# Performance work log

Measured on AMD Instinct MI355X. Metric: run time of the kernel, lower is better.

## Reference

```python
import jax, jax.numpy as jnp
import numpy as np

SIGMA_DATA = 16.0
ALPHA_BOND = 1.0


def safe_norm(x, axis=-1):
    # L2 norm with zero (sub)gradient at 0, matching torch.norm's behavior
    sq = jnp.sum(x * x, axis=axis)
    n = jnp.sqrt(jnp.where(sq > 0, sq, 1.0))
    return jnp.where(sq > 0, n, 0.0)


def weighted_rigid_align(x_l, xGT_l, w_l):
    # Aligns x_l onto xGT_l's frame (Kabsch with weights); output is detached.
    wm = w_l[..., None]                                   # [B,N,1]
    denom = jnp.sum(wm, axis=1, keepdims=True)
    mu = jnp.sum(wm * x_l, axis=1, keepdims=True) / denom
    muGT = jnp.sum(wm * xGT_l, axis=1, keepdims=True) / denom
    xc = x_l - mu
    xGTc = xGT_l - muGT
    # M = (w * xGT_c)^T @ x_c  -> [B,3,3]
    M = jnp.einsum('bni,bnj->bij', wm * xGTc, xc)
    U, S, Vh = jnp.linalg.svd(M)
    R = U @ Vh
    det = jnp.linalg.det(R)
    Fm = jnp.array([[1.0, 0.0, 0.0], [0.0, 1.0, 0.0], [0.0, 0.0, -1.0]], dtype=R.dtype)
    Rfix = jnp.einsum('bij,jk,bkl->bil', U, Fm, Vh)
    R = jnp.where(det[:, None, None] < 0, Rfix, R)
    xalign = xc @ jnp.swapaxes(R, -1, -2) + muGT
    return jax.lax.stop_gradient(xalign)


def diffusion_loss(xpred_l, xGT_l, ht, w_l):
    # Align ground truth onto prediction (note arg order in original forward)
    xGT_aligned = weighted_rigid_align(xGT_l, xpred_l, w_l)
    loss = jnp.sum(safe_norm(xpred_l - xGT_aligned) * w_l) / jnp.sum(w_l)
    if ALPHA_BOND > 0:
        w_pair = w_l[:, :, None] * w_l[:, None, :]                 # [B,N,N]
        d_pred = safe_norm(xpred_l[:, :, None] - xpred_l[:, None]) # [B,N,N]
        d_gt = safe_norm(xGT_l[:, :, None] - xGT_l[:, None])       # [B,N,N]
        L_bond = w_pair * (d_pred - d_gt) ** 2
        loss = loss + ALPHA_BOND * jnp.sum(L_bond) / jnp.sum(w_pair)
    return (ht ** 2 + SIGMA_DATA ** 2) / (ht + SIGMA_DATA) ** 2 * loss


def setup_inputs() -> dict:
    key = jax.random.key(0)
    k1, k2, k3, k4 = jax.random.split(key, 4)
    B, N = 4, 2048
    xpred_l = jax.random.normal(k1, (B, N, 3), dtype=jnp.float32) * 10.0
    xGT_l = jax.random.normal(k2, (B, N, 3), dtype=jnp.float32) * 10.0
    ht = jax.random.uniform(k3, (B,), dtype=jnp.float32, minval=0.1, maxval=4.0)
    w_l = jax.random.uniform(k4, (B, N), dtype=jnp.float32, minval=0.1, maxval=1.0)
    return {"xpred_l": xpred_l, "xGT_l": xGT_l, "ht": ht, "w_l": w_l}


def reference(xpred_l, xGT_l, ht, w_l):
    return diffusion_loss(xpred_l, xGT_l, ht, w_l)
```

## Files before the change

### kernel.cpp

```cpp
#include <hip/hip_runtime.h>
#include <math.h>


#define RT 256
#define CT 64
#define MAXB 8
#define MAXGX 16

__global__ __launch_bounds__(RT, 4)
void k_bond_stats(const float* __restrict__ pred, const float* __restrict__ gt,
                  const float* __restrict__ w, double* __restrict__ ws,
                  int N, int B) {
    const int b    = blockIdx.z;
    const int bx   = blockIdx.x;
    const int r0   = bx * RT;
    const int c0   = blockIdx.y * CT;
    const int tid  = threadIdx.x;
    const int lane = tid & 63, wave = tid >> 6;
    const int GX   = gridDim.x;
    const unsigned linear = (blockIdx.z * gridDim.y + blockIdx.y) * GX + blockIdx.x;

    double* statsSlot = ws;
    double* bondSlot  = ws + (size_t)B * GX * 16;

    const float* p  = pred + (size_t)b * N * 3;
    const float* g  = gt   + (size_t)b * N * 3;
    const float* wb = w    + (size_t)b * N;

    __shared__ float4 sp4[CT], sg4[CT];
    __shared__ double shred[4][16];

    const int  n      = r0 + tid;
    const bool row_ok = (n < N);
    float px=0.f,py=0.f,pz=0.f,gx=0.f,gy=0.f,gz=0.f,wn=0.f;
    if (row_ok) {
        px = p[3*n]; py = p[3*n+1]; pz = p[3*n+2];
        gx = g[3*n]; gy = g[3*n+1]; gz = g[3*n+2];
        wn = wb[n];
    }

    const bool bond_active = (c0 + CT > r0 + 1) && (c0 < N);
    float bond_f = 0.0f;
    if (bond_active) {
        for (int i = tid; i < CT; i += RT) {
            int m = c0 + i;
            float4 a = make_float4(0.f,0.f,0.f,0.f), c = a;
            if (m < N) {
                a = make_float4(p[3*m], p[3*m+1], p[3*m+2], wb[m]);
                c = make_float4(g[3*m], g[3*m+1], g[3*m+2], 0.f);
            }
            sp4[i] = a; sg4[i] = c;
        }
        __syncthreads();
        if (row_ok) {
            const int cc = min(CT, N - c0);
            if (c0 >= r0 + RT) {
                #pragma unroll 4
                for (int i = 0; i < cc; i++) {
                    float4 cp = sp4[i], cg = sg4[i];
                    float dxp=px-cp.x, dyp=py-cp.y, dzp=pz-cp.z;
                    float dxg=gx-cg.x, dyg=gy-cg.y, dzg=gz-cg.z;
                    float dp = sqrtf(dxp*dxp+dyp*dyp+dzp*dzp);
                    float dg = sqrtf(dxg*dxg+dyg*dyg+dzg*dzg);
                    float dd = dp - dg;
                    bond_f += (wn*cp.w)*(dd*dd);
                }
            } else if (n < c0 + cc - 1) {
                #pragma unroll 4
                for (int i = 0; i < cc; i++) {
                    float4 cp = sp4[i], cg = sg4[i];
                    float dxp=px-cp.x, dyp=py-cp.y, dzp=pz-cp.z;
                    float dxg=gx-cg.x, dyg=gy-cg.y, dzg=gz-cg.z;
                    float dp = sqrtf(dxp*dxp+dyp*dyp+dzp*dzp);
                    float dg = sqrtf(dxg*dxg+dyg*dyg+dzg*dzg);
                    float dd = dp - dg;
                    float t  = (wn*cp.w)*(dd*dd);
                    bond_f += (c0 + i > n) ? t : 0.0f;
                }
            }
        }
    }
    bond_f *= 2.0f;

    if (blockIdx.y == 0) {
        double wd=wn, pxd=px,pyd=py,pzd=pz, gxd=gx,gyd=gy,gzd=gz;
        double st[16] = {wd, wd*pxd, wd*pyd, wd*pzd, wd*gxd, wd*gyd, wd*gzd,
                         wd*pxd*gxd, wd*pxd*gyd, wd*pxd*gzd,
                         wd*pyd*gxd, wd*pyd*gyd, wd*pyd*gzd,
                         wd*pzd*gxd, wd*pzd*gyd, wd*pzd*gzd};
        #pragma unroll
        for (int off = 32; off > 0; off >>= 1) {
            #pragma unroll
            for (int k = 0; k < 16; k++) st[k] += __shfl_down(st[k], off, 64);
        }
        if (lane == 0) {
            #pragma unroll
            for (int k = 0; k < 16; k++) shred[wave][k] = st[k];
        }
        __syncthreads();
        if (tid < 16)
            statsSlot[((size_t)b*GX + bx)*16 + tid] =
                shred[0][tid]+shred[1][tid]+shred[2][tid]+shred[3][tid];
        __syncthreads();
    }

    double bd = (double)bond_f;
    #pragma unroll
    for (int off = 32; off > 0; off >>= 1) bd += __shfl_down(bd, off, 64);
    if (lane == 0) shred[wave][0] = bd;
    __syncthreads();
    if (tid == 0)
        bondSlot[linear] = shred[0][0]+shred[1][0]+shred[2][0]+shred[3][0];
}

__global__ __launch_bounds__(RT, 1)
void k_tail(const float* __restrict__ pred, const float* __restrict__ gt,
            const float* __restrict__ ht, const float* __restrict__ w,
            float* __restrict__ out, const double* __restrict__ ws,
            int N, int B, int GX, unsigned total) {
    const int tid  = threadIdx.x;
    const int lane = tid & 63, wave = tid >> 6;
    const double* statsSlot = ws;
    const double* bondSlot  = ws + (size_t)B * GX * 16;

    __shared__ double sstat[MAXB][16];
    __shared__ double shred[4][16];
    __shared__ float  Rf[MAXB][15];
    __shared__ double Wd[MAXB];
    __shared__ double s_bond, s_loss;

    if (tid < B * 16) {
        int bb = tid >> 4, k = tid & 15;
        double acc = 0.0;
        for (int j = 0; j < GX; j++) acc += statsSlot[((size_t)bb*GX + j)*16 + k];
        sstat[bb][k] = acc;
    }

    double bsum = 0.0;
    for (unsigned i = tid; i < total; i += RT) bsum += bondSlot[i];
    #pragma unroll
    for (int off = 32; off > 0; off >>= 1) bsum += __shfl_down(bsum, off, 64);
    if (lane == 0) shred[wave][0] = bsum;
    __syncthreads();
    if (tid == 0) s_bond = shred[0][0]+shred[1][0]+shred[2][0]+shred[3][0];

    if (tid < B) {
        const double* s = sstat[tid];
        double W = s[0];
        double mup[3] = { s[1]/W, s[2]/W, s[3]/W };
        double mug[3] = { s[4]/W, s[5]/W, s[6]/W };
        double M[3][3];
        for (int i = 0; i < 3; i++)
            for (int j = 0; j < 3; j++)
                M[i][j] = s[7 + i*3 + j] - W * mup[i] * mug[j];
        double A[3][3];
        for (int i = 0; i < 3; i++)
            for (int j = 0; j < 3; j++) {
                double t = 0.0;
                for (int k = 0; k < 3; k++) t += M[k][i] * M[k][j];
                A[i][j] = t;
            }
        double V[3][3] = {{1,0,0},{0,1,0},{0,0,1}};
        for (int sweep = 0; sweep < 6; sweep++) {
            for (int pq = 0; pq < 3; pq++) {
                int pp_ = (pq == 2) ? 1 : 0;
                int qq_ = (pq == 0) ? 1 : 2;
                double apq = A[pp_][qq_];
                if (fabs(apq) < 1e-300) continue;
                double app = A[pp_][pp_], aqq = A[qq_][qq_];
                double theta = (aqq - app) / (2.0 * apq);
                double t = copysign(1.0, theta) / (fabs(theta) + sqrt(theta*theta + 1.0));
                double cj = 1.0 / sqrt(t*t + 1.0), sn = t * cj;
                A[pp_][pp_] = app - t * apq;
                A[qq_][qq_] = aqq + t * apq;
                A[pp_][qq_] = A[qq_][pp_] = 0.0;
                int r = 3 - pp_ - qq_;
                double arp = A[r][pp_], arq = A[r][qq_];
                A[r][pp_] = A[pp_][r] = cj*arp - sn*arq;
                A[r][qq_] = A[qq_][r] = sn*arp + cj*arq;
                for (int rr = 0; rr < 3; rr++) {
                    double vp = V[rr][pp_], vq = V[rr][qq_];
                    V[rr][pp_] = cj*vp - sn*vq;
                    V[rr][qq_] = sn*vp + cj*vq;
                }
            }
        }
        double d[3] = { A[0][0], A[1][1], A[2][2] };
        int idx[3] = {0, 1, 2};
        for (int i = 0; i < 2; i++)
            for (int j = i + 1; j < 3; j++)
                if (d[idx[j]] > d[idx[i]]) { int tt = idx[i]; idx[i] = idx[j]; idx[j] = tt; }
        double u[3][3], v[3][3];
        for (int i = 0; i < 3; i++) {
            int c_ = idx[i];
            double sv = sqrt(fmax(d[c_], 0.0));
            double inv = (sv > 1e-12) ? 1.0 / sv : 0.0;
            for (int r = 0; r < 3; r++) v[i][r] = V[r][c_];
            for (int r = 0; r < 3; r++) {
                double t = 0.0;
                for (int k = 0; k < 3; k++) t += M[r][k] * v[i][k];
                u[i][r] = t * inv;
            }
        }
        double detM = M[0][0]*(M[1][1]*M[2][2] - M[1][2]*M[2][1])
                    - M[0][1]*(M[1][0]*M[2][2] - M[1][2]*M[2][0])
                    + M[0][2]*(M[1][0]*M[2][1] - M[1][1]*M[2][0]);
        double sg2 = (detM < 0.0) ? -1.0 : 1.0;
        for (int r = 0; r < 3; r++)
            for (int cc2 = 0; cc2 < 3; cc2++)
                Rf[tid][r*3+cc2] = (float)(u[0][r]*v[0][cc2] + u[1][r]*v[1][cc2]
                                           + sg2 * u[2][r]*v[2][cc2]);
        for (int i = 0; i < 3; i++) Rf[tid][9 + i]  = (float)mup[i];
        for (int i = 0; i < 3; i++) Rf[tid][12 + i] = (float)mug[i];
        Wd[tid] = W;
    }
    __syncthreads();

    double al = 0.0;
    for (int bb = 0; bb < B; bb++) {
        float R0=Rf[bb][0], R1=Rf[bb][1], R2=Rf[bb][2];
        float R3=Rf[bb][3], R4=Rf[bb][4], R5=Rf[bb][5];
        float R6=Rf[bb][6], R7=Rf[bb][7], R8=Rf[bb][8];
        float mp0=Rf[bb][9],  mp1=Rf[bb][10], mp2=Rf[bb][11];
        float mg0=Rf[bb][12], mg1=Rf[bb][13], mg2=Rf[bb][14];
        const float* pp  = pred + (size_t)bb * N * 3;
        const float* gg  = gt   + (size_t)bb * N * 3;
        const float* wwb = w    + (size_t)bb * N;
        for (int nn = tid; nn < N; nn += RT) {
            float x0 = gg[3*nn]-mg0, x1 = gg[3*nn+1]-mg1, x2 = gg[3*nn+2]-mg2;
            float ax = fmaf(R0,x0, fmaf(R1,x1, fmaf(R2,x2, mp0)));
            float ay = fmaf(R3,x0, fmaf(R4,x1, fmaf(R5,x2, mp1)));
            float az = fmaf(R6,x0, fmaf(R7,x1, fmaf(R8,x2, mp2)));
            float ex = pp[3*nn]-ax, ey = pp[3*nn+1]-ay, ez = pp[3*nn+2]-az;
            float sq = ex*ex + ey*ey + ez*ez;
            al += (double)(wwb[nn] * sqrtf(sq));
        }
    }
    #pragma unroll
    for (int off = 32; off > 0; off >>= 1) al += __shfl_down(al, off, 64);
    if (lane == 0) shred[wave][1] = al;
    __syncthreads();
    if (tid == 0) {
        double at = shred[0][1]+shred[1][1]+shred[2][1]+shred[3][1];
        double tw = 0.0, twp = 0.0;
        for (int i = 0; i < B; i++) { double W = Wd[i]; tw += W; twp += W*W; }
        s_loss = at / tw + s_bond / twp;
    }
    __syncthreads();
    if (tid < B) {
        double h = (double)ht[tid];
        out[tid] = (float)(((h*h + 256.0) / ((h + 16.0)*(h + 16.0))) * s_loss);
    }
}

extern "C" void kernel_launch(void* const* d_in, const int* in_sizes, int n_in,
                              void* d_out, int out_size, void* d_ws, size_t ws_size,
                              hipStream_t stream) {
    const float* pred = (const float*)d_in[0];
    const float* gt   = (const float*)d_in[1];
    const float* ht   = (const float*)d_in[2];
    const float* w    = (const float*)d_in[3];
    int B = in_sizes[2];
    int N = in_sizes[3] / B;
    double* ws = (double*)d_ws;
    float* out = (float*)d_out;

    int gx = (N + RT - 1) / RT;
    int gy = (N + CT - 1) / CT;
    unsigned total = (unsigned)(gx * gy * B);

    k_bond_stats<<<dim3(gx, gy, B), dim3(RT), 0, stream>>>(pred, gt, w, ws, N, B);
    k_tail<<<dim3(1), dim3(RT), 0, stream>>>(pred, gt, ht, w, out, ws, N, B, gx, total);
}
```

Baseline: 100.5 us.

## Fuse tail reduction into main kernel via last-block atomic counter

Merges the separate single-block tail kernel into the main bond/stats kernel: each block stores its partials with agent-scope atomic stores, then increments a global counter, and the last block to finish performs the Kabsch/SVD solve and the final alignment loss. This removes one kernel launch and the gap between kernels, but adds a memset launch to reset the counter. It also trims the Jacobi sweep count from 6 to 5. Ordering relies on relaxed atomics without explicit fences, which risks visibility issues, and the last block runs the serial tail while the rest of the GPU sits idle.

```diff
diff --git a/kernel.cpp b/kernel.cpp
--- a/kernel.cpp
+++ b/kernel.cpp
@@ -5,12 +5,12 @@
 #define RT 256
 #define CT 64
 #define MAXB 8
-#define MAXGX 16
 
 __global__ __launch_bounds__(RT, 4)
-void k_bond_stats(const float* __restrict__ pred, const float* __restrict__ gt,
-                  const float* __restrict__ w, double* __restrict__ ws,
-                  int N, int B) {
+void k_main(const float* __restrict__ pred, const float* __restrict__ gt,
+            const float* __restrict__ ht, const float* __restrict__ w,
+            float* __restrict__ out, double* __restrict__ ws,
+            int N, int B, unsigned total) {
     const int b    = blockIdx.z;
     const int bx   = blockIdx.x;
     const int r0   = bx * RT;
@@ -20,8 +20,9 @@
     const int GX   = gridDim.x;
     const unsigned linear = (blockIdx.z * gridDim.y + blockIdx.y) * GX + blockIdx.x;
 
-    double* statsSlot = ws;
-    double* bondSlot  = ws + (size_t)B * GX * 16;
+    double*   statsSlot = ws;
+    double*   bondSlot  = ws + (size_t)B * GX * 16;
+    unsigned* cnt       = (unsigned*)(bondSlot + total);
 
     const float* p  = pred + (size_t)b * N * 3;
     const float* g  = gt   + (size_t)b * N * 3;
@@ -99,8 +100,9 @@
         }
         __syncthreads();
         if (tid < 16)
-            statsSlot[((size_t)b*GX + bx)*16 + tid] =
-                shred[0][tid]+shred[1][tid]+shred[2][tid]+shred[3][tid];
+            __hip_atomic_store(&statsSlot[((size_t)b*GX + bx)*16 + tid],
+                               shred[0][tid]+shred[1][tid]+shred[2][tid]+shred[3][tid],
+                               __ATOMIC_RELAXED, __HIP_MEMORY_SCOPE_AGENT);
         __syncthreads();
     }
 
@@ -110,21 +112,18 @@
     if (lane == 0) shred[wave][0] = bd;
     __syncthreads();
     if (tid == 0)
-        bondSlot[linear] = shred[0][0]+shred[1][0]+shred[2][0]+shred[3][0];
-}
-
-__global__ __launch_bounds__(RT, 1)
-void k_tail(const float* __restrict__ pred, const float* __restrict__ gt,
-            const float* __restrict__ ht, const float* __restrict__ w,
-            float* __restrict__ out, const double* __restrict__ ws,
-            int N, int B, int GX, unsigned total) {
-    const int tid  = threadIdx.x;
-    const int lane = tid & 63, wave = tid >> 6;
-    const double* statsSlot = ws;
-    const double* bondSlot  = ws + (size_t)B * GX * 16;
+        __hip_atomic_store(&bondSlot[linear],
+                           shred[0][0]+shred[1][0]+shred[2][0]+shred[3][0],
+                           __ATOMIC_RELAXED, __HIP_MEMORY_SCOPE_AGENT);
+
+    __shared__ unsigned s_old;
+    __syncthreads();
+    if (tid == 0) s_old = __hip_atomic_fetch_add(cnt, 1u, __ATOMIC_RELAXED,
+                                                 __HIP_MEMORY_SCOPE_AGENT);
+    __syncthreads();
+    if (s_old != total - 1u) return;
 
     __shared__ double sstat[MAXB][16];
-    __shared__ double shred[4][16];
     __shared__ float  Rf[MAXB][15];
     __shared__ double Wd[MAXB];
     __shared__ double s_bond, s_loss;
@@ -132,17 +131,21 @@
     if (tid < B * 16) {
         int bb = tid >> 4, k = tid & 15;
         double acc = 0.0;
-        for (int j = 0; j < GX; j++) acc += statsSlot[((size_t)bb*GX + j)*16 + k];
+        for (int j = 0; j < GX; j++)
+            acc += __hip_atomic_load(&statsSlot[((size_t)bb*GX + j)*16 + k],
+                                     __ATOMIC_RELAXED, __HIP_MEMORY_SCOPE_AGENT);
         sstat[bb][k] = acc;
     }
 
     double bsum = 0.0;
-    for (unsigned i = tid; i < total; i += RT) bsum += bondSlot[i];
+    for (unsigned i = tid; i < total; i += RT)
+        bsum += __hip_atomic_load(&bondSlot[i], __ATOMIC_RELAXED,
+                                  __HIP_MEMORY_SCOPE_AGENT);
     #pragma unroll
     for (int off = 32; off > 0; off >>= 1) bsum += __shfl_down(bsum, off, 64);
-    if (lane == 0) shred[wave][0] = bsum;
-    __syncthreads();
-    if (tid == 0) s_bond = shred[0][0]+shred[1][0]+shred[2][0]+shred[3][0];
+    if (lane == 0) shred[wave][1] = bsum;
+    __syncthreads();
+    if (tid == 0) s_bond = shred[0][1]+shred[1][1]+shred[2][1]+shred[3][1];
 
     if (tid < B) {
         const double* s = sstat[tid];
@@ -161,7 +164,7 @@
                 A[i][j] = t;
             }
         double V[3][3] = {{1,0,0},{0,1,0},{0,0,1}};
-        for (int sweep = 0; sweep < 6; sweep++) {
+        for (int sweep = 0; sweep < 5; sweep++) {
             for (int pq = 0; pq < 3; pq++) {
                 int pp_ = (pq == 2) ? 1 : 0;
                 int qq_ = (pq == 0) ? 1 : 2;
@@ -238,10 +241,10 @@
     }
     #pragma unroll
     for (int off = 32; off > 0; off >>= 1) al += __shfl_down(al, off, 64);
-    if (lane == 0) shred[wave][1] = al;
+    if (lane == 0) shred[wave][2] = al;
     __syncthreads();
     if (tid == 0) {
-        double at = shred[0][1]+shred[1][1]+shred[2][1]+shred[3][1];
+        double at = shred[0][2]+shred[1][2]+shred[2][2]+shred[3][2];
         double tw = 0.0, twp = 0.0;
         for (int i = 0; i < B; i++) { double W = Wd[i]; tw += W; twp += W*W; }
         s_loss = at / tw + s_bond / twp;
@@ -268,7 +271,8 @@
     int gx = (N + RT - 1) / RT;
     int gy = (N + CT - 1) / CT;
     unsigned total = (unsigned)(gx * gy * B);
-
-    k_bond_stats<<<dim3(gx, gy, B), dim3(RT), 0, stream>>>(pred, gt, w, ws, N, B);
-    k_tail<<<dim3(1), dim3(RT), 0, stream>>>(pred, gt, ht, w, out, ws, N, B, gx, total);
+    size_t cnt_off = ((size_t)B * gx * 16 + total) * sizeof(double);
+
+    hipMemsetAsync((char*)d_ws + cnt_off, 0, sizeof(unsigned), stream);
+    k_main<<<dim3(gx, gy, B), dim3(RT), 0, stream>>>(pred, gt, ht, w, out, ws, N, B, total);
 }
```

New measurement: 100.7 us. Within noise of the previous version (+0.2%).
